# Performance work log

Hardware: AMD Instinct MI355X
Metric: run time of the kernel (lower is better)

## Reference

```python
import jax, jax.numpy as jnp
import numpy as np


def setup_inputs() -> dict:
    key = jax.random.key(0)
    kx, kw = jax.random.split(key)
    # x: [batch, seq, in_features]
    x = jax.random.normal(kx, (4, 2048, 4096), dtype=jnp.float32)
    # packed uint8-style weight: [(out_features+3)//4, in_features] = [4096, 4096]
    weight = jax.random.randint(kw, (4096, 4096), 0, 256, dtype=jnp.int32)
    return {"x": x, "weight": weight}


def reference(x, weight):
    # Faithful to BitLinear.forward: cast packed weight to x.dtype, then F.linear
    # (no unpacking, no weight_scale applied, bias disabled -> omitted).
    w = weight.astype(x.dtype)  # [packed_out, in]
    # y[b,s,o] = sum_d x[b,s,d] * w[o,d]
    y = jnp.einsum("bsd,od->bso", x, w)
    return y
```

## Files before the change

kernel.cpp:

```cpp
#include <hip/hip_runtime.h>


typedef __bf16 bf16x8 __attribute__((ext_vector_type(8)));
typedef float f32x4 __attribute__((ext_vector_type(4)));
typedef unsigned short u16;
typedef u16 u16x8 __attribute__((ext_vector_type(8)));

__device__ __forceinline__ u16 f2bf(float f) {
    unsigned int u = __builtin_bit_cast(unsigned int, f);
    u = (u + 0x7FFFu + ((u >> 16) & 1u)) >> 16;
    return (u16)u;
}

__global__ void cvt_f32_bf16_k(const float* __restrict__ in, u16* __restrict__ out, int nvec) {
    int i = blockIdx.x * blockDim.x + threadIdx.x;
    if (i >= nvec) return;
    const float4* p = (const float4*)in;
    float4 a = p[2 * i];
    float4 b = p[2 * i + 1];
    u16x8 o;
    o[0] = f2bf(a.x); o[1] = f2bf(a.y); o[2] = f2bf(a.z); o[3] = f2bf(a.w);
    o[4] = f2bf(b.x); o[5] = f2bf(b.y); o[6] = f2bf(b.z); o[7] = f2bf(b.w);
    *(u16x8*)(out + 8 * (size_t)i) = o;
}

__global__ void cvt_i32_bf16_k(const int* __restrict__ in, u16* __restrict__ out, int nvec) {
    int i = blockIdx.x * blockDim.x + threadIdx.x;
    if (i >= nvec) return;
    const int4* p = (const int4*)in;
    int4 a = p[2 * i];
    int4 b = p[2 * i + 1];
    u16x8 o;
    o[0] = f2bf((float)a.x); o[1] = f2bf((float)a.y); o[2] = f2bf((float)a.z); o[3] = f2bf((float)a.w);
    o[4] = f2bf((float)b.x); o[5] = f2bf((float)b.y); o[6] = f2bf((float)b.z); o[7] = f2bf((float)b.w);
    *(u16x8*)(out + 8 * (size_t)i) = o;
}

#define GLD_LDS16(gp, lp)                                                     \
    __builtin_amdgcn_global_load_lds(                                         \
        (const __attribute__((address_space(1))) void*)(gp),                  \
        (__attribute__((address_space(3))) void*)(lp), 16, 0, 0)

#define BM 128
#define BN 128
#define BK 32

__global__ void gemm_bf16_bt(const u16* __restrict__ A, const u16* __restrict__ B,
                             float* __restrict__ C, int M, int N, int K) {
    __shared__ u16 As[BM * BK];
    __shared__ u16 Bs[BN * BK];

    const int tid  = threadIdx.x;
    const int lane = tid & 63;
    const int wid  = tid >> 6;
    const int wr   = wid >> 1;
    const int wc   = wid & 1;

    const int nwg = gridDim.x;
    const int cpx = nwg >> 3;
    const int bid = blockIdx.x;
    const int swz = (bid & 7) * cpx + (bid >> 3);

    const int tiles_n = N / BN;
    const int tm = swz / tiles_n;
    const int tn = swz % tiles_n;
    const int row0 = tm * BM;
    const int col0 = tn * BN;

    const int srow  = wid * 32 + (lane >> 2);
    const int skoff = (lane & 3) * 8;

    const u16* Ap0 = A + (size_t)(row0 + srow) * K + skoff;
    const u16* Ap1 = A + (size_t)(row0 + srow + 16) * K + skoff;
    const u16* Bp0 = B + (size_t)(col0 + srow) * K + skoff;
    const u16* Bp1 = B + (size_t)(col0 + srow + 16) * K + skoff;

    u16* As0 = &As[(wid * 32) * BK];
    u16* As1 = &As[(wid * 32 + 16) * BK];
    u16* Bs0 = &Bs[(wid * 32) * BK];
    u16* Bs1 = &Bs[(wid * 32 + 16) * BK];

    f32x4 acc[4][4] = {};

    const int fr = lane & 15;
    const int fk = (lane >> 4) * 8;

    for (int kt = 0; kt < K; kt += BK) {
        GLD_LDS16(Ap0, As0);
        GLD_LDS16(Ap1, As1);
        GLD_LDS16(Bp0, Bs0);
        GLD_LDS16(Bp1, Bs1);
        Ap0 += BK; Ap1 += BK; Bp0 += BK; Bp1 += BK;
        __syncthreads();

        bf16x8 af[4], bfr[4];
#pragma unroll
        for (int m = 0; m < 4; ++m)
            af[m] = *(const bf16x8*)&As[(wr * 64 + m * 16 + fr) * BK + fk];
#pragma unroll
        for (int n = 0; n < 4; ++n)
            bfr[n] = *(const bf16x8*)&Bs[(wc * 64 + n * 16 + fr) * BK + fk];

#pragma unroll
        for (int m = 0; m < 4; ++m)
#pragma unroll
            for (int n = 0; n < 4; ++n)
                acc[m][n] = __builtin_amdgcn_mfma_f32_16x16x32_bf16(af[m], bfr[n], acc[m][n], 0, 0, 0);

        __syncthreads();
    }

    const int crow = (lane >> 4) * 4;
    const int ccol = lane & 15;
#pragma unroll
    for (int m = 0; m < 4; ++m) {
#pragma unroll
        for (int n = 0; n < 4; ++n) {
            const size_t base = (size_t)(row0 + wr * 64 + m * 16 + crow) * N
                              + (col0 + wc * 64 + n * 16 + ccol);
#pragma unroll
            for (int r = 0; r < 4; ++r)
                C[base + (size_t)r * N] = acc[m][n][r];
        }
    }
}

extern "C" void kernel_launch(void* const* d_in, const int* in_sizes, int n_in,
                              void* d_out, int out_size, void* d_ws, size_t ws_size,
                              hipStream_t stream) {
    const float* x = (const float*)d_in[0];
    const int*   w = (const int*)d_in[1];
    float*     out = (float*)d_out;

    const int M = 8192, N = 4096, K = 4096;

    u16* xb = (u16*)d_ws;
    u16* wb = xb + (size_t)M * K;

    {
        int nvec = (M * K) / 8;
        cvt_f32_bf16_k<<<dim3(nvec / 256), dim3(256), 0, stream>>>(x, xb, nvec);
    }
    {
        int nvec = (N * K) / 8;
        cvt_i32_bf16_k<<<dim3(nvec / 256), dim3(256), 0, stream>>>(w, wb, nvec);
    }

    dim3 grid((M / BM) * (N / BN));
    gemm_bf16_bt<<<grid, dim3(256), 0, stream>>>(xb, wb, out, M, N, K);
}
```

Baseline: 583.5 us.

## Rewrite GEMM as 256x256 8-wave pipelined kernel and fuse conversion kernels

Replaces the 128x128 single-buffered GEMM with a 256x256 tile, 512-thread kernel that double-buffers 64-wide K chunks in LDS and splits each iteration into eight phases interleaving global-to-LDS loads with MFMA work. It adds an XOR swizzle on the LDS layout to avoid bank conflicts and raises wave priority during the MFMA bursts. The two dtype conversion kernels are merged into one grid-stride kernel. The pipeline relies on K being a power of two (wraparound mask) and on hand-placed vmcnt waits, and it uses 128KB of LDS per block.

```diff
diff --git a/kernel.cpp b/kernel.cpp
--- a/kernel.cpp
+++ b/kernel.cpp
@@ -12,115 +12,145 @@
     return (u16)u;
 }
 
-__global__ void cvt_f32_bf16_k(const float* __restrict__ in, u16* __restrict__ out, int nvec) {
-    int i = blockIdx.x * blockDim.x + threadIdx.x;
-    if (i >= nvec) return;
-    const float4* p = (const float4*)in;
-    float4 a = p[2 * i];
-    float4 b = p[2 * i + 1];
-    u16x8 o;
-    o[0] = f2bf(a.x); o[1] = f2bf(a.y); o[2] = f2bf(a.z); o[3] = f2bf(a.w);
-    o[4] = f2bf(b.x); o[5] = f2bf(b.y); o[6] = f2bf(b.z); o[7] = f2bf(b.w);
-    *(u16x8*)(out + 8 * (size_t)i) = o;
+__global__ void cvt_fused_k(const float* __restrict__ x, const int* __restrict__ w,
+                            u16* __restrict__ xb, u16* __restrict__ wb,
+                            int nxv, int nwv) {
+    const int stride = gridDim.x * blockDim.x;
+    for (int i = blockIdx.x * blockDim.x + threadIdx.x; i < nxv + nwv; i += stride) {
+        if (i < nxv) {
+            const float4* p = (const float4*)x;
+            float4 a = p[2 * (size_t)i];
+            float4 b = p[2 * (size_t)i + 1];
+            u16x8 o;
+            o[0] = f2bf(a.x); o[1] = f2bf(a.y); o[2] = f2bf(a.z); o[3] = f2bf(a.w);
+            o[4] = f2bf(b.x); o[5] = f2bf(b.y); o[6] = f2bf(b.z); o[7] = f2bf(b.w);
+            *(u16x8*)(xb + 8 * (size_t)i) = o;
+        } else {
+            int j = i - nxv;
+            const int4* p = (const int4*)w;
+            int4 a = p[2 * (size_t)j];
+            int4 b = p[2 * (size_t)j + 1];
+            u16x8 o;
+            o[0] = f2bf((float)a.x); o[1] = f2bf((float)a.y); o[2] = f2bf((float)a.z); o[3] = f2bf((float)a.w);
+            o[4] = f2bf((float)b.x); o[5] = f2bf((float)b.y); o[6] = f2bf((float)b.z); o[7] = f2bf((float)b.w);
+            *(u16x8*)(wb + 8 * (size_t)j) = o;
+        }
+    }
 }
 
-__global__ void cvt_i32_bf16_k(const int* __restrict__ in, u16* __restrict__ out, int nvec) {
-    int i = blockIdx.x * blockDim.x + threadIdx.x;
-    if (i >= nvec) return;
-    const int4* p = (const int4*)in;
-    int4 a = p[2 * i];
-    int4 b = p[2 * i + 1];
-    u16x8 o;
-    o[0] = f2bf((float)a.x); o[1] = f2bf((float)a.y); o[2] = f2bf((float)a.z); o[3] = f2bf((float)a.w);
-    o[4] = f2bf((float)b.x); o[5] = f2bf((float)b.y); o[6] = f2bf((float)b.z); o[7] = f2bf((float)b.w);
-    *(u16x8*)(out + 8 * (size_t)i) = o;
-}
 
-#define GLD_LDS16(gp, lp)                                                     \
-    __builtin_amdgcn_global_load_lds(                                         \
-        (const __attribute__((address_space(1))) void*)(gp),                  \
-        (__attribute__((address_space(3))) void*)(lp), 16, 0, 0)
+#define STAGE(SBUF, SMAT, SKH, SKT)                                            \
+    {                                                                          \
+        const u16* gb = ((SMAT) == 0) ? Ab : Bb;                               \
+        _Pragma("unroll")                                                      \
+        for (int j = 0; j < 2; ++j) {                                          \
+            const int c = wid * 2 + j;                                         \
+            const u16* src = gb + (size_t)(c * 16 + srow) * K                  \
+                             + (SKT) + (SKH) * 32 + ssig;                      \
+            __builtin_amdgcn_global_load_lds(                                  \
+                (const __attribute__((address_space(1))) void*)src,            \
+                (__attribute__((address_space(3))) void*)(                     \
+                    lds + (((SBUF) * 2 + (SMAT)) * 2 + (SKH)) * 8192 + c * 512), \
+                16, 0, 0);                                                     \
+        }                                                                      \
+    }
 
-#define BM 128
-#define BN 128
-#define BK 32
+#define PHASE(PBUF, CH, KH, SBUF, SMAT, SKH, SKT, DOVM)                        \
+    {                                                                          \
+        if ((CH) == 0) {                                                       \
+            _Pragma("unroll")                                                  \
+            for (int n = 0; n < 4; ++n)                                        \
+                bfrag[n] = *(const bf16x8*)((const char*)lds                   \
+                    + (((PBUF) * 2 + 1) * 2 + (KH)) * 16384                    \
+                    + (wc * 64 + n * 16 + fr) * 64 + rd_sl);                   \
+        }                                                                      \
+        bf16x8 afrag[4];                                                       \
+        _Pragma("unroll")                                                      \
+        for (int mi = 0; mi < 4; ++mi)                                         \
+            afrag[mi] = *(const bf16x8*)((const char*)lds                      \
+                + (((PBUF) * 2 + 0) * 2 + (KH)) * 16384                        \
+                + (wr * 128 + ((CH) * 4 + mi) * 16 + fr) * 64 + rd_sl);        \
+        STAGE(SBUF, SMAT, SKH, SKT);                                           \
+        if (DOVM) asm volatile("s_waitcnt vmcnt(4)" ::: "memory");             \
+        asm volatile("s_barrier" ::: "memory");                                \
+        __builtin_amdgcn_s_setprio(1);                                         \
+        _Pragma("unroll")                                                      \
+        for (int mi = 0; mi < 4; ++mi)                                         \
+            _Pragma("unroll")                                                  \
+            for (int n = 0; n < 4; ++n)                                        \
+                acc[(CH) * 4 + mi][n] = __builtin_amdgcn_mfma_f32_16x16x32_bf16( \
+                    afrag[mi], bfrag[n], acc[(CH) * 4 + mi][n], 0, 0, 0);      \
+        __builtin_amdgcn_s_setprio(0);                                         \
+        asm volatile("s_barrier" ::: "memory");                                \
+    }
 
-__global__ void gemm_bf16_bt(const u16* __restrict__ A, const u16* __restrict__ B,
-                             float* __restrict__ C, int M, int N, int K) {
-    __shared__ u16 As[BM * BK];
-    __shared__ u16 Bs[BN * BK];
+__global__ __launch_bounds__(512, 2)
+void gemm_bf16_8ph(const u16* __restrict__ A, const u16* __restrict__ B,
+                   float* __restrict__ C, int M, int N, int K) {
+    __shared__ u16 lds[65536];
 
     const int tid  = threadIdx.x;
     const int lane = tid & 63;
     const int wid  = tid >> 6;
-    const int wr   = wid >> 1;
-    const int wc   = wid & 1;
+    const int wr   = wid >> 2;
+    const int wc   = wid & 3;
+    const int fr   = lane & 15;
+    const int g    = lane >> 4;
 
     const int nwg = gridDim.x;
     const int cpx = nwg >> 3;
     const int bid = blockIdx.x;
     const int swz = (bid & 7) * cpx + (bid >> 3);
+    const int tiles_n = N / 256;
+    const int row0 = (swz / tiles_n) * 256;
+    const int col0 = (swz % tiles_n) * 256;
 
-    const int tiles_n = N / BN;
-    const int tm = swz / tiles_n;
-    const int tn = swz % tiles_n;
-    const int row0 = tm * BM;
-    const int col0 = tn * BN;
+    const int srow = lane >> 2;
+    const int ssig = (((lane & 3) ^ ((lane >> 2) & 3))) * 8;
 
-    const int srow  = wid * 32 + (lane >> 2);
-    const int skoff = (lane & 3) * 8;
+    const u16* Ab = A + (size_t)row0 * K;
+    const u16* Bb = B + (size_t)col0 * K;
 
-    const u16* Ap0 = A + (size_t)(row0 + srow) * K + skoff;
-    const u16* Ap1 = A + (size_t)(row0 + srow + 16) * K + skoff;
-    const u16* Bp0 = B + (size_t)(col0 + srow) * K + skoff;
-    const u16* Bp1 = B + (size_t)(col0 + srow + 16) * K + skoff;
+    const int rd_sl = (g ^ (fr & 3)) << 4;
 
-    u16* As0 = &As[(wid * 32) * BK];
-    u16* As1 = &As[(wid * 32 + 16) * BK];
-    u16* Bs0 = &Bs[(wid * 32) * BK];
-    u16* Bs1 = &Bs[(wid * 32 + 16) * BK];
+    f32x4 acc[8][4] = {};
+    bf16x8 bfrag[4];
 
-    f32x4 acc[4][4] = {};
+    STAGE(0, 0, 0, 0);
+    STAGE(0, 1, 0, 0);
+    STAGE(0, 0, 1, 0);
+    STAGE(0, 1, 1, 0);
+    STAGE(1, 0, 0, 64);
+    STAGE(1, 1, 0, 64);
+    asm volatile("s_waitcnt vmcnt(4)" ::: "memory");
+    asm volatile("s_barrier" ::: "memory");
 
-    const int fr = lane & 15;
-    const int fk = (lane >> 4) * 8;
-
-    for (int kt = 0; kt < K; kt += BK) {
-        GLD_LDS16(Ap0, As0);
-        GLD_LDS16(Ap1, As1);
-        GLD_LDS16(Bp0, Bs0);
-        GLD_LDS16(Bp1, Bs1);
-        Ap0 += BK; Ap1 += BK; Bp0 += BK; Bp1 += BK;
-        __syncthreads();
-
-        bf16x8 af[4], bfr[4];
-#pragma unroll
-        for (int m = 0; m < 4; ++m)
-            af[m] = *(const bf16x8*)&As[(wr * 64 + m * 16 + fr) * BK + fk];
-#pragma unroll
-        for (int n = 0; n < 4; ++n)
-            bfr[n] = *(const bf16x8*)&Bs[(wc * 64 + n * 16 + fr) * BK + fk];
-
-#pragma unroll
-        for (int m = 0; m < 4; ++m)
-#pragma unroll
-            for (int n = 0; n < 4; ++n)
-                acc[m][n] = __builtin_amdgcn_mfma_f32_16x16x32_bf16(af[m], bfr[n], acc[m][n], 0, 0, 0);
-
-        __syncthreads();
+    const int KMASK = K - 1;
+    int kt = 0;
+    for (int i = 0; i < K / 128; ++i) {
+        const int k2 = (kt + 128) & KMASK;
+        const int k3 = (kt + 192) & KMASK;
+        PHASE(0, 0, 0,  1, 0, 1, kt + 64, false);
+        PHASE(0, 1, 0,  1, 1, 1, kt + 64, false);
+        PHASE(0, 0, 1,  0, 0, 0, k2,      false);
+        PHASE(0, 1, 1,  0, 1, 0, k2,      true);
+        PHASE(1, 0, 0,  0, 0, 1, k2,      false);
+        PHASE(1, 1, 0,  0, 1, 1, k2,      false);
+        PHASE(1, 0, 1,  1, 0, 0, k3,      false);
+        PHASE(1, 1, 1,  1, 1, 0, k3,      true);
+        kt += 128;
     }
 
-    const int crow = (lane >> 4) * 4;
-    const int ccol = lane & 15;
+    const int crow0 = row0 + wr * 128 + g * 4;
+    const int ccol0 = col0 + wc * 64 + fr;
 #pragma unroll
-    for (int m = 0; m < 4; ++m) {
+    for (int mf = 0; mf < 8; ++mf) {
 #pragma unroll
         for (int n = 0; n < 4; ++n) {
-            const size_t base = (size_t)(row0 + wr * 64 + m * 16 + crow) * N
-                              + (col0 + wc * 64 + n * 16 + ccol);
+            const size_t base = (size_t)(crow0 + mf * 16) * N + ccol0 + n * 16;
 #pragma unroll
             for (int r = 0; r < 4; ++r)
-                C[base + (size_t)r * N] = acc[m][n][r];
+                C[base + (size_t)r * N] = acc[mf][n][r];
         }
     }
 }
@@ -138,14 +168,11 @@
     u16* wb = xb + (size_t)M * K;
 
     {
-        int nvec = (M * K) / 8;
-        cvt_f32_bf16_k<<<dim3(nvec / 256), dim3(256), 0, stream>>>(x, xb, nvec);
-    }
-    {
-        int nvec = (N * K) / 8;
-        cvt_i32_bf16_k<<<dim3(nvec / 256), dim3(256), 0, stream>>>(w, wb, nvec);
+        int nxv = (M * K) / 8;
+        int nwv = (N * K) / 8;
+        cvt_fused_k<<<dim3(4096), dim3(256), 0, stream>>>(x, w, xb, wb, nxv, nwv);
     }
 
-    dim3 grid((M / BM) * (N / BN));
-    gemm_bf16_bt<<<grid, dim3(256), 0, stream>>>(xb, wb, out, M, N, K);
+    dim3 grid((M / 256) * (N / 256));
+    gemm_bf16_8ph<<<grid, dim3(512), 0, stream>>>(xb, wb, out, M, N, K);
 }
```

After: 509.9 us. 1.14x faster.
